# Kernel tuning notes

Measured on AMD Instinct MI355X. Metric: run time of the kernel, lower is better.

The kernel has to match this reference:

```python
import jax, jax.numpy as jnp
import numpy as np

B, C, H, W = 1, 128, 48, 48
HC = 32                     # head_channel
NH = C // HC                # num heads = 4
K = 16                      # n_clusters
N = H * W                   # 2304
SCALE = HC ** 0.5
EPS = 1e-6


def setup_inputs() -> dict:
    key = jax.random.key(0)
    ks = jax.random.split(key, 20)
    s = 0.05  # weight init scale ~ xavier-ish for C=128
    def g(i, shape, sc=s):
        return jax.random.normal(ks[i], shape, dtype=jnp.float32) * sc
    return {
        'q_img': g(0, (B, C, H, W), 1.0),
        'k_img_map': g(1, (B, C, H, W), 1.0),
        'v_img_map': g(2, (B, C, H, W), 1.0),
        'pixel_coefficients': jax.random.uniform(ks[3], (B, N, N), dtype=jnp.float32),
        'labels': jax.random.randint(ks[4], (B, H, W), 0, K),
        # projections (stored as [in, out]; y = x @ w + b)
        'wq': g(5, (C, C)), 'bq': jnp.zeros((C,), jnp.float32),
        'wk': g(6, (C, C)), 'bk': jnp.zeros((C,), jnp.float32),
        'wv': g(7, (C, C)), 'bv': jnp.zeros((C,), jnp.float32),
        # mlp_1: Linear(C,2C) -> LeakyReLU(0.01) -> Linear(2C,C) (dropout=0 -> identity)
        'w1a': g(8, (C, 2 * C)), 'b1a': jnp.zeros((2 * C,), jnp.float32),
        'w1b': g(9, (2 * C, C)), 'b1b': jnp.zeros((C,), jnp.float32),
        # mlp_2
        'w2a': g(10, (C, 2 * C)), 'b2a': jnp.zeros((2 * C,), jnp.float32),
        'w2b': g(11, (2 * C, C)), 'b2b': jnp.zeros((C,), jnp.float32),
    }


def _mlp(x, wa, ba, wb, bb):
    h = x @ wa + ba
    h = jax.nn.leaky_relu(h, negative_slope=0.01)
    return h @ wb + bb


def reference(q_img, k_img_map, v_img_map, pixel_coefficients,
              wq, bq, wk, bk, wv, bv,
              w1a, b1a, w1b, b1b, w2a, b2a, w2b, b2b,
              labels):
    # projections on channel-last pixels
    q = q_img.transpose(0, 2, 3, 1).reshape(B, N, C) @ wq + bq
    k = k_img_map.transpose(0, 2, 3, 1).reshape(B, N, C) @ wk + bk
    v = v_img_map.transpose(0, 2, 3, 1).reshape(B, N, C) @ wv + bv

    labels_flat = labels.reshape(B, N)
    onehot = jax.nn.one_hot(labels_flat, K, dtype=q.dtype)        # [B,N,K]
    num_k = jnp.einsum('bnk,bnc->bkc', onehot, k)                 # [B,K,C]
    den_k = onehot.sum(axis=1)[:, :, None] + EPS                  # [B,K,1]
    centers_k = num_k / den_k

    qm = q.reshape(B, N, NH, HC).transpose(0, 2, 1, 3)            # [B,h,N,d]
    km = k.reshape(B, N, NH, HC).transpose(0, 2, 1, 3)
    vm = v.reshape(B, N, NH, HC).transpose(0, 2, 1, 3)
    kcm = centers_k.reshape(B, K, NH, HC).transpose(0, 2, 1, 3)   # [B,h,K,d]

    attn_intra = jnp.einsum('bhid,bhjd->bhij', qm, km)            # [B,h,N,N]
    attn_centers = jnp.einsum('bhid,bhkd->bhik', qm, kcm)         # [B,h,N,K]

    # gather center score per key's cluster: attn_centers[b,h,i,labels[b,j]]
    idx = jnp.broadcast_to(labels_flat[:, None, None, :], (B, NH, N, N))
    attn_inter = jnp.take_along_axis(attn_centers, idx, axis=3)   # [B,h,N,N]
    attn_inter = attn_inter * pixel_coefficients[:, None, :, :]

    same = labels_flat[:, None, :, None] == labels_flat[:, None, None, :]  # [B,1,N,N]
    scores = jnp.where(same, attn_intra, attn_inter) / SCALE
    attn_w = jax.nn.softmax(scores, axis=-1)

    out = jnp.einsum('bhij,bhjd->bhid', attn_w, vm)
    out = out.transpose(0, 2, 1, 3).reshape(B, N, C)              # [B,N,C]

    v_spatial = v.reshape(B, H, W, C).transpose(0, 3, 1, 2)       # [B,C,H,W]
    rs1 = v_spatial + _mlp(out, w1a, b1a, w1b, b1b).transpose(0, 2, 1).reshape(B, C, H, W)
    rs1_flat = rs1.transpose(0, 2, 3, 1).reshape(B, N, C)
    rs2 = rs1 + _mlp(rs1_flat, w2a, b2a, w2b, b2b).transpose(0, 2, 1).reshape(B, C, H, W)
    return rs2
```

## Files before the change

kernel.cpp:

```cpp
#include <hip/hip_runtime.h>
#include <hip/hip_bf16.h>
#include <math.h>

#define NPIX 2304
#define CCH  128
#define NH   4
#define HC   32
#define NCL  16
#define KSPLIT 8
#define KEYS 288
#define NSTEP 9
#define QSCALE 0.25503489f

typedef __attribute__((ext_vector_type(8))) short short8;
typedef __attribute__((ext_vector_type(4))) short short4v;
typedef __attribute__((ext_vector_type(4))) float f32x4;

#if __has_builtin(__builtin_amdgcn_exp2f)
#define EXP2(x) __builtin_amdgcn_exp2f(x)
#else
#define EXP2(x) __expf((x) * 0.6931471805599453f)
#endif

static __device__ __forceinline__ short f2bf(float x) {
    __hip_bfloat16 b = __float2bfloat16(x);
    return *reinterpret_cast<short*>(&b);
}

__global__ void __launch_bounds__(256) pack_w_kernel(
        const float* __restrict__ wq,  const float* __restrict__ wk,
        const float* __restrict__ wv,
        const float* __restrict__ w1a, const float* __restrict__ w1b,
        const float* __restrict__ w2a, const float* __restrict__ w2b,
        short* __restrict__ tq,  short* __restrict__ tk,
        short* __restrict__ tv,
        short* __restrict__ t1a, short* __restrict__ t1b,
        short* __restrict__ t2a, short* __restrict__ t2b) {
    const int idx = blockIdx.x * 256 + threadIdx.x;
    if (idx < 16384) {
        const int sel = idx >> 12, local = idx & 4095;
        short8 s;
        if (sel == 0 || sel == 2) {
            const float* src = (sel == 0) ? w1a : w2a;
            short*       dst = (sel == 0) ? t1a : t2a;
            const int o = local >> 4, g = local & 15;
#pragma unroll
            for (int j = 0; j < 8; ++j) s[j] = f2bf(src[(g * 8 + j) * 256 + o]);
            *(short8*)(dst + (size_t)o * 128 + g * 8) = s;
        } else {
            const float* src = (sel == 1) ? w1b : w2b;
            short*       dst = (sel == 1) ? t1b : t2b;
            const int o = local >> 5, g = local & 31;
#pragma unroll
            for (int j = 0; j < 8; ++j) s[j] = f2bf(src[(g * 8 + j) * 128 + o]);
            *(short8*)(dst + (size_t)o * 256 + g * 8) = s;
        }
    } else if (idx < 22528) {
        const int i2 = idx - 16384;
        const int sel = i2 >> 11, local = i2 & 2047;
        const float* src = (sel == 0) ? wq : (sel == 1) ? wk : wv;
        short*       dst = (sel == 0) ? tq : (sel == 1) ? tk : tv;
        const int o = local >> 4, g = local & 15;
        short8 s;
#pragma unroll
        for (int j = 0; j < 8; ++j) s[j] = f2bf(src[(g * 8 + j) * 128 + o]);
        *(short8*)(dst + (size_t)o * 128 + g * 8) = s;
    }
}

__global__ void __launch_bounds__(256) proj_kernel(
        const float* __restrict__ xq, const float* __restrict__ xk,
        const float* __restrict__ xv, const int* __restrict__ labels,
        const short* __restrict__ tq, const float* __restrict__ bq,
        const short* __restrict__ tk, const float* __restrict__ bk,
        const short* __restrict__ tv, const float* __restrict__ bv,
        short* __restrict__ qbf, short* __restrict__ kbf,
        float* __restrict__ vbuf, short* __restrict__ vbfT,
        float* __restrict__ cpart, float* __restrict__ denpart) {
    __shared__ __align__(16) short xbf[16 * 136];
    __shared__ float kf[16 * 128];
    __shared__ float ls2[2 * NCL * CCH];
    __shared__ float smls[32];
    const int which = blockIdx.y;
    const int pxblk = blockIdx.x;
    const int t  = threadIdx.x;

    const int n0 = pxblk * 16;
    const int w    = t >> 6;
    const int lane = t & 63;
    const int quad = lane >> 4;
    const int lq   = lane & 15;
    const float* x  = (which == 0) ? xq : (which == 1) ? xk : xv;
    const short* wt = (which == 0) ? tq : (which == 1) ? tk : tv;
    const float* b  = (which == 0) ? bq : (which == 1) ? bk : bv;

#pragma unroll
    for (int it = 0; it < 8; ++it) {
        const int flat = it * 256 + t;
        const int cc = flat >> 4, p = flat & 15;
        xbf[p * 136 + cc] = f2bf(x[cc * NPIX + n0 + p]);
    }
    if (which == 1)
        for (int u = t; u < 2 * NCL * CCH; u += 256) ls2[u] = 0.f;
    __syncthreads();

    short8 a[4];
#pragma unroll
    for (int ks = 0; ks < 4; ++ks)
        a[ks] = *(const short8*)(xbf + lq * 136 + ks * 32 + quad * 8);

    float ov[2][4];
#pragma unroll
    for (int tile = 0; tile < 2; ++tile) {
        const int out0 = w * 32 + tile * 16;
        f32x4 acc = {0.f, 0.f, 0.f, 0.f};
#pragma unroll
        for (int ks = 0; ks < 4; ++ks) {
            const short8 bw = *(const short8*)(wt + (size_t)(out0 + lq) * 128 + ks * 32 + quad * 8);
            acc = __builtin_amdgcn_mfma_f32_16x16x32_bf16(a[ks], bw, acc, 0, 0, 0);
        }
        const float bb = b[out0 + lq];
#pragma unroll
        for (int r = 0; r < 4; ++r) ov[tile][r] = acc[r] + bb;
    }

    if (which == 0) {
#pragma unroll
        for (int tile = 0; tile < 2; ++tile)
#pragma unroll
            for (int r = 0; r < 4; ++r)
                qbf[(size_t)(n0 + quad * 4 + r) * CCH + w * 32 + tile * 16 + lq] =
                    f2bf(ov[tile][r] * QSCALE);
    } else if (which == 1) {
#pragma unroll
        for (int tile = 0; tile < 2; ++tile)
#pragma unroll
            for (int r = 0; r < 4; ++r) {
                const float v = ov[tile][r];
                const int out0 = w * 32 + tile * 16;
                kbf[(size_t)(n0 + quad * 4 + r) * CCH + out0 + lq] = f2bf(v);
                kf[(quad * 4 + r) * 128 + out0 + lq] = v;
            }
        __syncthreads();
        const int c = t & 127, ph = t >> 7;
        int lab8[8];
#pragma unroll
        for (int p = 0; p < 8; ++p) lab8[p] = labels[n0 + ph * 8 + p];
#pragma unroll
        for (int p = 0; p < 8; ++p)
            ls2[(ph * NCL + lab8[p]) * CCH + c] += kf[(ph * 8 + p) * 128 + c];
        if (t < 32) {
            const int g2 = t >> 4, cl = t & 15;
            int cnt = 0;
#pragma unroll
            for (int p = 0; p < 8; ++p)
                cnt += (labels[n0 + g2 * 8 + p] == cl) ? 1 : 0;
            smls[t] = (float)cnt;
        }
        __syncthreads();
        for (int u = t; u < NCL * CCH; u += 256)
            cpart[(size_t)pxblk * 2048 + u] = ls2[u] + ls2[2048 + u];
        if (t < 16)
            denpart[pxblk * 16 + t] = smls[t] + smls[16 + t];
    } else {
#pragma unroll
        for (int tile = 0; tile < 2; ++tile)
#pragma unroll
            for (int r = 0; r < 4; ++r) {
                const float v = ov[tile][r];
                const int out0 = w * 32 + tile * 16;
                vbuf[(size_t)(n0 + quad * 4 + r) * CCH + out0 + lq] = v;
                vbfT[(size_t)(out0 + lq) * NPIX + n0 + quad * 4 + r] = f2bf(v);
            }
    }
}

__global__ void centersB_kernel(const float* __restrict__ cpart,
                                const float* __restrict__ denpart,
                                short* __restrict__ cbf) {
    const int idx = blockIdx.x * 256 + threadIdx.x;
    const int kk  = idx >> 7;
    float den = 0.f, s = 0.f;
    for (int b = 0; b < 144; ++b) den += denpart[b * 16 + kk];
    for (int b = 0; b < 144; ++b) s   += cpart[(size_t)b * 2048 + idx];
    cbf[idx] = f2bf(s / (den + 1e-6f));
}

__global__ void __launch_bounds__(256, 4) attn_part_kernel(
        const short* __restrict__ qbf,  const short* __restrict__ kbf,
        const short* __restrict__ vbfT, const short* __restrict__ cbf,
        const int* __restrict__ labels, const float* __restrict__ pc,
        float* __restrict__ part_o, float* __restrict__ part_l) {
    __shared__ __align__(16) short Pl[NH][16 * 40];
    __shared__ __align__(16) float aclT[NH][16][16];
    __shared__ int   labl[KEYS];
    const int qt   = blockIdx.x;
    const int ks   = blockIdx.y;
    const int tid  = threadIdx.x;
    const int w    = tid >> 6;
    const int lane = tid & 63;
    const int quad = lane >> 4;
    const int lq   = lane & 15;
    const int i0   = qt * 16;
    const int j0   = ks * KEYS;

    for (int u = tid; u < KEYS / 4; u += 256)
        *(int4*)(labl + u * 4) = *(const int4*)(labels + j0 + u * 4);

    const short8 aq = *(const short8*)(qbf + (size_t)(i0 + lq) * CCH + w * HC + quad * 8);
    {
        const short8 bc = *(const short8*)(cbf + (size_t)lq * CCH + w * HC + quad * 8);
        f32x4 z = {0.f, 0.f, 0.f, 0.f};
        f32x4 acd = __builtin_amdgcn_mfma_f32_16x16x32_bf16(aq, bc, z, 0, 0, 0);
        *(f32x4*)(&aclT[w][lq][quad * 4]) = acd;
    }
    int labi[4];
#pragma unroll
    for (int r = 0; r < 4; ++r) labi[r] = labels[i0 + quad * 4 + r];

    __syncthreads();

    const short* kp  = kbf  + (size_t)(j0 + lq) * CCH + w * HC + quad * 8;
    const short* vp  = vbfT + (size_t)(w * HC + lq) * NPIX + j0 + quad * 8;
    const float* pcp = pc   + (size_t)(i0 + quad * 4) * NPIX + j0 + lq;

    short8 k0A, k1A, v0A, v1A, k0B, k1B, v0B, v1B;
    float pcA[8], pcB[8];
    f32x4 accO0 = {0.f, 0.f, 0.f, 0.f};
    f32x4 accO1 = {0.f, 0.f, 0.f, 0.f};
    float lp[4] = {0.f, 0.f, 0.f, 0.f};

#define ISSUE(K0_, K1_, V0_, V1_, s) do {                                         \
        K0_ = *(const short8*)(kp + (size_t)(s) * 32 * CCH);                      \
        K1_ = *(const short8*)(kp + (size_t)((s) * 32 + 16) * CCH);               \
        V0_ = *(const short8*)(vp + (s) * 32);                                    \
        V1_ = *(const short8*)(vp + (size_t)16 * NPIX + (s) * 32);                \
    } while (0)

#define ISSUE_PC(dst, s) do {                                                     \
        _Pragma("unroll")                                                         \
        for (int r_ = 0; r_ < 4; ++r_) {                                          \
            dst[r_ * 2 + 0] = pcp[(size_t)r_ * NPIX + (s) * 32];                  \
            dst[r_ * 2 + 1] = pcp[(size_t)r_ * NPIX + (s) * 32 + 16];             \
        }                                                                         \
    } while (0)

#define COMPUTE(s, K0_, K1_, V0_, V1_, PCUSE) do {                                \
        _Pragma("unroll")                                                         \
        for (int kh = 0; kh < 2; ++kh) {                                          \
            const short8 bk = (kh == 0) ? K0_ : K1_;                              \
            f32x4 z = {0.f, 0.f, 0.f, 0.f};                                       \
            const f32x4 sv = __builtin_amdgcn_mfma_f32_16x16x32_bf16(aq, bk, z, 0, 0, 0);\
            const int slab = labl[(s) * 32 + kh * 16 + lq];                       \
            const f32x4 av4 = *(const f32x4*)(&aclT[w][slab][quad * 4]);          \
            _Pragma("unroll")                                                     \
            for (int r = 0; r < 4; ++r) {                                         \
                const float sc_ = (slab == labi[r]) ? sv[r] : av4[r] * PCUSE[r * 2 + kh];\
                const float p   = EXP2(sc_);                                      \
                lp[r] += p;                                                       \
                Pl[w][(quad * 4 + r) * 40 + kh * 16 + lq] = f2bf(p);              \
            }                                                                     \
        }                                                                         \
        const short8 ap = *(const short8*)(&Pl[w][lq * 40 + quad * 8]);           \
        accO0 = __builtin_amdgcn_mfma_f32_16x16x32_bf16(ap, V0_, accO0, 0, 0, 0); \
        accO1 = __builtin_amdgcn_mfma_f32_16x16x32_bf16(ap, V1_, accO1, 0, 0, 0); \
    } while (0)

    ISSUE(k0A, k1A, v0A, v1A, 0);
    ISSUE_PC(pcA, 0);
    for (int sb = 0; sb < NSTEP; sb += 2) {
        if (sb + 1 < NSTEP) { ISSUE(k0B, k1B, v0B, v1B, sb + 1); ISSUE_PC(pcB, sb + 1); }
        COMPUTE(sb, k0A, k1A, v0A, v1A, pcA);
        if (sb + 1 < NSTEP) {
            if (sb + 2 < NSTEP) { ISSUE(k0A, k1A, v0A, v1A, sb + 2); ISSUE_PC(pcA, sb + 2); }
            COMPUTE(sb + 1, k0B, k1B, v0B, v1B, pcB);
        }
    }
#undef ISSUE
#undef ISSUE_PC
#undef COMPUTE

#pragma unroll
    for (int r = 0; r < 4; ++r) {
        float v = lp[r];
        v += __shfl_xor(v, 1, 64);
        v += __shfl_xor(v, 2, 64);
        v += __shfl_xor(v, 4, 64);
        v += __shfl_xor(v, 8, 64);
        lp[r] = v;
    }
    if (lq == 0) {
#pragma unroll
        for (int r = 0; r < 4; ++r)
            part_l[((size_t)ks * NPIX + i0 + quad * 4 + r) * NH + w] = lp[r];
    }
#pragma unroll
    for (int r = 0; r < 4; ++r) {
        float* po = part_o + ((size_t)ks * NPIX + i0 + quad * 4 + r) * CCH + w * HC;
        po[lq]      = accO0[r];
        po[16 + lq] = accO1[r];
    }
}

#define XS 136
#define HS 264
__global__ void __launch_bounds__(256) mlp_mfma_kernel(
        const float* __restrict__ part_o, const float* __restrict__ part_l,
        const float* __restrict__ vbuf,
        const short* __restrict__ t1a, const float* __restrict__ b1a,
        const short* __restrict__ t1b, const float* __restrict__ b1b,
        const short* __restrict__ t2a, const float* __restrict__ b2a,
        const short* __restrict__ t2b, const float* __restrict__ b2b,
        float* __restrict__ outp) {
    __shared__ __align__(16) short xbf[16 * XS];
    __shared__ __align__(16) short hbf[16 * HS];
    __shared__ __align__(16) short r1bf[16 * XS];
    __shared__ float fT[128 * 20];
    const int n0 = blockIdx.x * 16;
    const int t  = threadIdx.x;
    const int w  = t >> 6, lane = t & 63, quad = lane >> 4, lq = lane & 15;

    for (int u = t; u < 512; u += 256) {
        const int p = u >> 5, c4 = (u & 31) * 4, hh = c4 >> 5;
        float ls_ = 0.f;
#pragma unroll
        for (int ks = 0; ks < KSPLIT; ++ks)
            ls_ += part_l[((size_t)ks * NPIX + n0 + p) * NH + hh];
        float sx = 0.f, sy = 0.f, sz = 0.f, sw2 = 0.f;
#pragma unroll
        for (int ks = 0; ks < KSPLIT; ++ks) {
            const float4 v = *(const float4*)(part_o + ((size_t)ks * NPIX + n0 + p) * CCH + c4);
            sx += v.x; sy += v.y; sz += v.z; sw2 += v.w;
        }
        const float inv = 1.f / ls_;
        short4v s;
        s[0] = f2bf(sx * inv); s[1] = f2bf(sy * inv);
        s[2] = f2bf(sz * inv); s[3] = f2bf(sw2 * inv);
        *(short4v*)(xbf + p * XS + c4) = s;
    }
    __syncthreads();

    {
        short8 a[4];
#pragma unroll
        for (int ks = 0; ks < 4; ++ks)
            a[ks] = *(const short8*)(xbf + lq * XS + ks * 32 + quad * 8);
#pragma unroll
        for (int tile = 0; tile < 4; ++tile) {
            const int out0 = w * 64 + tile * 16;
            f32x4 acc = {0.f, 0.f, 0.f, 0.f};
#pragma unroll
            for (int ks = 0; ks < 4; ++ks) {
                const short8 b = *(const short8*)(t1a + (size_t)(out0 + lq) * 128 + ks * 32 + quad * 8);
                acc = __builtin_amdgcn_mfma_f32_16x16x32_bf16(a[ks], b, acc, 0, 0, 0);
            }
            const float bb = b1a[out0 + lq];
#pragma unroll
            for (int r = 0; r < 4; ++r) {
                float v = acc[r] + bb;
                v = (v > 0.f) ? v : 0.01f * v;
                hbf[(quad * 4 + r) * HS + out0 + lq] = f2bf(v);
            }
        }
    }
    __syncthreads();

    float rs1f[2][4];
    {
        short8 a[8];
#pragma unroll
        for (int ks = 0; ks < 8; ++ks)
            a[ks] = *(const short8*)(hbf + lq * HS + ks * 32 + quad * 8);
#pragma unroll
        for (int tile = 0; tile < 2; ++tile) {
            const int out0 = w * 32 + tile * 16;
            f32x4 acc = {0.f, 0.f, 0.f, 0.f};
#pragma unroll
            for (int ks = 0; ks < 8; ++ks) {
                const short8 b = *(const short8*)(t1b + (size_t)(out0 + lq) * 256 + ks * 32 + quad * 8);
                acc = __builtin_amdgcn_mfma_f32_16x16x32_bf16(a[ks], b, acc, 0, 0, 0);
            }
            const float bb = b1b[out0 + lq];
#pragma unroll
            for (int r = 0; r < 4; ++r) {
                const float v = acc[r] + bb +
                    vbuf[(size_t)(n0 + quad * 4 + r) * CCH + out0 + lq];
                rs1f[tile][r] = v;
                r1bf[(quad * 4 + r) * XS + out0 + lq] = f2bf(v);
            }
        }
    }
    __syncthreads();

    {
        short8 a[4];
#pragma unroll
        for (int ks = 0; ks < 4; ++ks)
            a[ks] = *(const short8*)(r1bf + lq * XS + ks * 32 + quad * 8);
#pragma unroll
        for (int tile = 0; tile < 4; ++tile) {
            const int out0 = w * 64 + tile * 16;
            f32x4 acc = {0.f, 0.f, 0.f, 0.f};
#pragma unroll
            for (int ks = 0; ks < 4; ++ks) {
                const short8 b = *(const short8*)(t2a + (size_t)(out0 + lq) * 128 + ks * 32 + quad * 8);
                acc = __builtin_amdgcn_mfma_f32_16x16x32_bf16(a[ks], b, acc, 0, 0, 0);
            }
            const float bb = b2a[out0 + lq];
#pragma unroll
            for (int r = 0; r < 4; ++r) {
                float v = acc[r] + bb;
                v = (v > 0.f) ? v : 0.01f * v;
                hbf[(quad * 4 + r) * HS + out0 + lq] = f2bf(v);
            }
        }
    }
    __syncthreads();

    {
        short8 a[8];
#pragma unroll
        for (int ks = 0; ks < 8; ++ks)
            a[ks] = *(const short8*)(hbf + lq * HS + ks * 32 + quad * 8);
#pragma unroll
        for (int tile = 0; tile < 2; ++tile) {
            const int out0 = w * 32 + tile * 16;
            f32x4 acc = {0.f, 0.f, 0.f, 0.f};
#pragma unroll
            for (int ks = 0; ks < 8; ++ks) {
                const short8 b = *(const short8*)(t2b + (size_t)(out0 + lq) * 256 + ks * 32 + quad * 8);
                acc = __builtin_amdgcn_mfma_f32_16x16x32_bf16(a[ks], b, acc, 0, 0, 0);
            }
            const float bb = b2b[out0 + lq];
#pragma unroll
            for (int r = 0; r < 4; ++r)
                fT[(out0 + lq) * 20 + quad * 4 + r] = acc[r] + bb + rs1f[tile][r];
        }
    }
    __syncthreads();

    for (int u = t; u < 512; u += 256) {
        const int row = u >> 2, seg = u & 3;
        const float4 v = *(const float4*)(fT + row * 20 + seg * 4);
        *(float4*)(outp + (size_t)row * NPIX + n0 + seg * 4) = v;
    }
}

extern "C" void kernel_launch(void* const* d_in, const int* in_sizes, int n_in,
                              void* d_out, int out_size, void* d_ws, size_t ws_size,
                              hipStream_t stream) {
    const float* q_img = (const float*)d_in[0];
    const float* k_img = (const float*)d_in[1];
    const float* v_img = (const float*)d_in[2];
    const float* pc    = (const float*)d_in[3];
    const int*   labels= (const int*)  d_in[4];
    const float* wq = (const float*)d_in[5];   const float* bq = (const float*)d_in[6];
    const float* wk = (const float*)d_in[7];   const float* bk = (const float*)d_in[8];
    const float* wv = (const float*)d_in[9];   const float* bv = (const float*)d_in[10];
    const float* w1a = (const float*)d_in[11]; const float* b1a = (const float*)d_in[12];
    const float* w1b = (const float*)d_in[13]; const float* b1b = (const float*)d_in[14];
    const float* w2a = (const float*)d_in[15]; const float* b2a = (const float*)d_in[16];
    const float* w2b = (const float*)d_in[17]; const float* b2b = (const float*)d_in[18];

    float* fw = (float*)d_ws;
    float* vbuf    = fw;
    float* part_o  = vbuf + (size_t)NPIX * CCH;
    float* part_l  = part_o + (size_t)KSPLIT * NPIX * CCH;
    float* cpart   = part_l + (size_t)KSPLIT * NPIX * NH;
    float* denpart = cpart + (size_t)144 * 2048;
    short* t1a  = (short*)(denpart + 144 * 16);
    short* t1b  = t1a + 32768;
    short* t2a  = t1b + 32768;
    short* t2b  = t2a + 32768;
    short* tq   = t2b + 32768;
    short* tk   = tq + 16384;
    short* tv   = tk + 16384;
    short* qbf  = tv + 16384;
    short* kbf  = qbf + (size_t)NPIX * CCH;
    short* vbfT = kbf + (size_t)NPIX * CCH;
    short* cbf  = vbfT + (size_t)NPIX * CCH;

    pack_w_kernel<<<88, 256, 0, stream>>>(
        wq, wk, wv, w1a, w1b, w2a, w2b, tq, tk, tv, t1a, t1b, t2a, t2b);
    proj_kernel<<<dim3(144, 3), 256, 0, stream>>>(
        q_img, k_img, v_img, labels, tq, bq, tk, bk, tv, bv,
        qbf, kbf, vbuf, vbfT, cpart, denpart);
    centersB_kernel<<<8, 256, 0, stream>>>(cpart, denpart, cbf);
    attn_part_kernel<<<dim3(144, KSPLIT), 256, 0, stream>>>(
        qbf, kbf, vbfT, cbf, labels, pc, part_o, part_l);
    mlp_mfma_kernel<<<144, 256, 0, stream>>>(
        part_o, part_l, vbuf, t1a, b1a, t1b, b1b, t2a, b2a, t2b, b2b,
        (float*)d_out);
}
```

Before: 155.9 us.

## Software-pipeline QK softmax and PV MFMA stages across key steps

Splits each key step into a QK/exp stage and a PV MFMA stage, and runs PV for step s-1 after QK for step s. This lets the PV matrix multiply overlap with the next step's score computation. The P tile in LDS is now double-buffered and V registers are triple-buffered to support the skew, and the loop is fully unrolled. The cost is more LDS and VGPRs, which could hurt occupancy under launch_bounds(256,4).

```diff
diff --git a/kernel.cpp b/kernel.cpp
--- a/kernel.cpp
+++ b/kernel.cpp
@@ -191,7 +191,7 @@
         const short* __restrict__ vbfT, const short* __restrict__ cbf,
         const int* __restrict__ labels, const float* __restrict__ pc,
         float* __restrict__ part_o, float* __restrict__ part_l) {
-    __shared__ __align__(16) short Pl[NH][16 * 40];
+    __shared__ __align__(16) short Pl[NH][2][16 * 40];
     __shared__ __align__(16) float aclT[NH][16][16];
     __shared__ int   labl[KEYS];
     const int qt   = blockIdx.x;
@@ -224,17 +224,21 @@
     const short* vp  = vbfT + (size_t)(w * HC + lq) * NPIX + j0 + quad * 8;
     const float* pcp = pc   + (size_t)(i0 + quad * 4) * NPIX + j0 + lq;
 
-    short8 k0A, k1A, v0A, v1A, k0B, k1B, v0B, v1B;
+    short8 kA0, kA1, kB0, kB1;
+    short8 v0s[3], v1s[3];
     float pcA[8], pcB[8];
     f32x4 accO0 = {0.f, 0.f, 0.f, 0.f};
     f32x4 accO1 = {0.f, 0.f, 0.f, 0.f};
     float lp[4] = {0.f, 0.f, 0.f, 0.f};
 
-#define ISSUE(K0_, K1_, V0_, V1_, s) do {                                         \
+#define ISSUE_K(K0_, K1_, s) do {                                                 \
         K0_ = *(const short8*)(kp + (size_t)(s) * 32 * CCH);                      \
         K1_ = *(const short8*)(kp + (size_t)((s) * 32 + 16) * CCH);               \
-        V0_ = *(const short8*)(vp + (s) * 32);                                    \
-        V1_ = *(const short8*)(vp + (size_t)16 * NPIX + (s) * 32);                \
+    } while (0)
+
+#define ISSUE_V(slot, s) do {                                                     \
+        v0s[slot] = *(const short8*)(vp + (s) * 32);                              \
+        v1s[slot] = *(const short8*)(vp + (size_t)16 * NPIX + (s) * 32);          \
     } while (0)
 
 #define ISSUE_PC(dst, s) do {                                                     \
@@ -245,7 +249,7 @@
         }                                                                         \
     } while (0)
 
-#define COMPUTE(s, K0_, K1_, V0_, V1_, PCUSE) do {                                \
+#define QK(s, K0_, K1_, PCUSE, pb) do {                                           \
         _Pragma("unroll")                                                         \
         for (int kh = 0; kh < 2; ++kh) {                                          \
             const short8 bk = (kh == 0) ? K0_ : K1_;                              \
@@ -258,27 +262,37 @@
                 const float sc_ = (slab == labi[r]) ? sv[r] : av4[r] * PCUSE[r * 2 + kh];\
                 const float p   = EXP2(sc_);                                      \
                 lp[r] += p;                                                       \
-                Pl[w][(quad * 4 + r) * 40 + kh * 16 + lq] = f2bf(p);              \
+                Pl[w][pb][(quad * 4 + r) * 40 + kh * 16 + lq] = f2bf(p);          \
             }                                                                     \
         }                                                                         \
-        const short8 ap = *(const short8*)(&Pl[w][lq * 40 + quad * 8]);           \
-        accO0 = __builtin_amdgcn_mfma_f32_16x16x32_bf16(ap, V0_, accO0, 0, 0, 0); \
-        accO1 = __builtin_amdgcn_mfma_f32_16x16x32_bf16(ap, V1_, accO1, 0, 0, 0); \
     } while (0)
 
-    ISSUE(k0A, k1A, v0A, v1A, 0);
+#define PV(pb, vslot) do {                                                        \
+        const short8 ap = *(const short8*)(&Pl[w][pb][lq * 40 + quad * 8]);       \
+        accO0 = __builtin_amdgcn_mfma_f32_16x16x32_bf16(ap, v0s[vslot], accO0, 0, 0, 0);\
+        accO1 = __builtin_amdgcn_mfma_f32_16x16x32_bf16(ap, v1s[vslot], accO1, 0, 0, 0);\
+    } while (0)
+
+    ISSUE_K(kA0, kA1, 0);
     ISSUE_PC(pcA, 0);
-    for (int sb = 0; sb < NSTEP; sb += 2) {
-        if (sb + 1 < NSTEP) { ISSUE(k0B, k1B, v0B, v1B, sb + 1); ISSUE_PC(pcB, sb + 1); }
-        COMPUTE(sb, k0A, k1A, v0A, v1A, pcA);
+    ISSUE_V(0, 0);
+#pragma unroll
+    for (int sb = 0; sb < NSTEP; ++sb) {
         if (sb + 1 < NSTEP) {
-            if (sb + 2 < NSTEP) { ISSUE(k0A, k1A, v0A, v1A, sb + 2); ISSUE_PC(pcA, sb + 2); }
-            COMPUTE(sb + 1, k0B, k1B, v0B, v1B, pcB);
-        }
-    }
-#undef ISSUE
+            if ((sb & 1) == 0) { ISSUE_K(kB0, kB1, sb + 1); ISSUE_PC(pcB, sb + 1); }
+            else               { ISSUE_K(kA0, kA1, sb + 1); ISSUE_PC(pcA, sb + 1); }
+            ISSUE_V((sb + 1) % 3, sb + 1);
+        }
+        if ((sb & 1) == 0) QK(sb, kA0, kA1, pcA, 0);
+        else               QK(sb, kB0, kB1, pcB, 1);
+        if (sb > 0) PV((sb - 1) & 1, (sb - 1) % 3);
+    }
+    PV((NSTEP - 1) & 1, (NSTEP - 1) % 3);
+#undef ISSUE_K
+#undef ISSUE_V
 #undef ISSUE_PC
-#undef COMPUTE
+#undef QK
+#undef PV
 
 #pragma unroll
     for (int r = 0; r < 4; ++r) {
```

Result: no change. 153.5 us (-1.6%).
